# Kernel tuning notes

Measured on AMD Instinct MI355X. Metric: run time of the kernel, lower is better.

## Reference

```python
import jax, jax.numpy as jnp
import numpy as np

N = 100000   # nodes
E = 1000000  # edges per block
P = 100000   # pos/neg link edges
IN = 128
H = 64


def setup_inputs() -> dict:
    key = jax.random.key(0)
    ks = jax.random.split(key, 24)
    d = {}
    d["x"] = jax.random.normal(ks[0], (N, IN), jnp.float32)
    d["edge_weight"] = jax.random.uniform(ks[1], (3, E), jnp.float32)
    d["src"] = jax.random.randint(ks[2], (E,), 0, N)
    d["dst"] = jax.random.randint(ks[3], (E,), 0, N)
    d["pos_src"] = jax.random.randint(ks[4], (P,), 0, N)
    d["pos_dst"] = jax.random.randint(ks[5], (P,), 0, N)
    d["neg_src"] = jax.random.randint(ks[6], (P,), 0, N)
    d["neg_dst"] = jax.random.randint(ks[7], (P,), 0, N)
    s = 1.0 / np.sqrt(IN)
    h = 1.0 / np.sqrt(H)
    d["W0"] = jax.random.normal(ks[8], (IN, H), jnp.float32) * s
    d["b0"] = jnp.zeros((H,), jnp.float32)
    d["W1"] = jax.random.normal(ks[9], (H, H), jnp.float32) * h
    d["b1"] = jnp.zeros((H,), jnp.float32)
    d["W2"] = jax.random.normal(ks[10], (H, H), jnp.float32) * h
    d["b2"] = jnp.zeros((H,), jnp.float32)
    d["P0"] = jax.random.normal(ks[11], (H, H), jnp.float32) * h
    d["pb0"] = jnp.zeros((H,), jnp.float32)
    d["P1"] = jax.random.normal(ks[12], (H, H), jnp.float32) * h
    d["pb1"] = jnp.zeros((H,), jnp.float32)
    d["P2"] = jax.random.normal(ks[13], (H, 1), jnp.float32) * h
    d["pb2"] = jnp.zeros((1,), jnp.float32)
    return d


def _graph_conv(h, W, b, src, dst, ew, n_nodes):
    # DGL GraphConv, norm='both': D_out^{-1/2} on source feats,
    # edge-weighted sum aggregation, D_in^{-1/2} on result, then linear.
    ones = jnp.ones(src.shape[0], h.dtype)
    deg_out = jax.ops.segment_sum(ones, src, num_segments=n_nodes)
    deg_in = jax.ops.segment_sum(ones, dst, num_segments=n_nodes)
    norm_src = jax.lax.rsqrt(jnp.maximum(deg_out, 1.0))
    norm_dst = jax.lax.rsqrt(jnp.maximum(deg_in, 1.0))
    # apply weight before aggregation (in_feats >= out_feats); math-equivalent either way
    hw = (h * norm_src[:, None]) @ W            # [N, H]
    msg = hw[src] * ew[:, None]                 # [E, H] gather + scale
    agg = jax.ops.segment_sum(msg, dst, num_segments=n_nodes)  # scatter-add
    return agg * norm_dst[:, None] + b


def reference(x, edge_weight, src, dst, pos_src, pos_dst, neg_src, neg_dst,
              W0, b0, W1, b1, W2, b2, P0, pb0, P1, pb1, P2, pb2):
    h = jax.nn.relu(_graph_conv(x, W0, b0, src, dst, edge_weight[0], N))
    h = jax.nn.relu(_graph_conv(h, W1, b1, src, dst, edge_weight[1], N))
    h = _graph_conv(h, W2, b2, src, dst, edge_weight[2], N)  # no relu on last layer

    def mlp(z):
        z = jax.nn.relu(z @ P0 + pb0)
        z = jax.nn.relu(z @ P1 + pb1)
        return z @ P2 + pb2

    h_pos = mlp(h[pos_src] * h[pos_dst])  # [P, 1]
    h_neg = mlp(h[neg_src] * h[neg_dst])  # [P, 1]
    return (h_pos, h_neg)
```

## Files before the change

### kernel.cpp

```cpp
#include <hip/hip_runtime.h>


#define NN 100000
#define NE 1000000
#define NP 100000
#define SCAN_NB 98

__device__ __forceinline__ void row_fma(float4& acc, float xv, const float4& wv) {
    acc.x = fmaf(xv, wv.x, acc.x);
    acc.y = fmaf(xv, wv.y, acc.y);
    acc.z = fmaf(xv, wv.z, acc.z);
    acc.w = fmaf(xv, wv.w, acc.w);
}

__global__ void deg_kernel(const int4* __restrict__ src4, const int4* __restrict__ dst4,
                           int* __restrict__ deg_out, int* __restrict__ deg_in, int E4) {
    int tid = blockIdx.x * blockDim.x + threadIdx.x;
    if (tid < E4) {
        int4 s = src4[tid], d = dst4[tid];
        atomicAdd(&deg_out[s.x], 1);
        atomicAdd(&deg_out[s.y], 1);
        atomicAdd(&deg_out[s.z], 1);
        atomicAdd(&deg_out[s.w], 1);
        atomicAdd(&deg_in[d.x], 1);
        atomicAdd(&deg_in[d.y], 1);
        atomicAdd(&deg_in[d.z], 1);
        atomicAdd(&deg_in[d.w], 1);
    }
}

__global__ void norm_kernel(const int* __restrict__ deg_out, const int* __restrict__ deg_in,
                            float* __restrict__ norm_src, float* __restrict__ norm_dst, int n) {
    int i = blockIdx.x * blockDim.x + threadIdx.x;
    if (i < n) {
        norm_src[i] = rsqrtf(fmaxf((float)deg_out[i], 1.0f));
        norm_dst[i] = rsqrtf(fmaxf((float)deg_in[i], 1.0f));
    }
}

__global__ __launch_bounds__(1024) void scan_block(const int* __restrict__ deg,
                                                   int* __restrict__ tmp_excl,
                                                   int* __restrict__ blocksums, int n) {
    __shared__ int wsums[16];
    const int i = blockIdx.x * 1024 + threadIdx.x;
    const int lane = threadIdx.x & 63, w = threadIdx.x >> 6;
    int v = (i < n) ? deg[i] : 0;
    int s = v;
#pragma unroll
    for (int off = 1; off < 64; off <<= 1) {
        int u = __shfl_up(s, off, 64);
        if (lane >= off) s += u;
    }
    if (lane == 63) wsums[w] = s;
    __syncthreads();
    if (w == 0) {
        int wv = (lane < 16) ? wsums[lane] : 0;
#pragma unroll
        for (int off = 1; off < 16; off <<= 1) {
            int u = __shfl_up(wv, off, 64);
            if (lane >= off) wv += u;
        }
        if (lane < 16) wsums[lane] = wv;
    }
    __syncthreads();
    int excl = s - v + (w > 0 ? wsums[w - 1] : 0);
    if (i < n) tmp_excl[i] = excl;
    if (threadIdx.x == 1023) blocksums[blockIdx.x] = excl + v;
}

__global__ void scan_sums(int* __restrict__ bs, int nb) {
    __shared__ int wtot[2];
    const int t = threadIdx.x;
    const int lane = t & 63, w = t >> 6;
    int v = (t < nb) ? bs[t] : 0;
    int s = v;
#pragma unroll
    for (int off = 1; off < 64; off <<= 1) {
        int u = __shfl_up(s, off, 64);
        if (lane >= off) s += u;
    }
    if (lane == 63) wtot[w] = s;
    __syncthreads();
    int excl = s - v + (w == 1 ? wtot[0] : 0);
    if (t < nb) bs[t] = excl;
}

__global__ __launch_bounds__(1024) void scan_apply(const int* __restrict__ tmp_excl,
                                                   const int* __restrict__ bs,
                                                   int* __restrict__ row_ptr,
                                                   int* __restrict__ cursor, int n) {
    const int i = blockIdx.x * 1024 + threadIdx.x;
    if (i < n) {
        int r = tmp_excl[i] + bs[blockIdx.x];
        row_ptr[i] = r;
        cursor[i] = r;
    }
    if (i == 0) row_ptr[n] = NE;
}

__global__ void csr_fill(const int* __restrict__ src, const int* __restrict__ dst,
                         const float* __restrict__ ew, int* __restrict__ cursor,
                         float4* __restrict__ cedge, int E) {
    int tid = blockIdx.x * blockDim.x + threadIdx.x;
    int stride = gridDim.x * blockDim.x;
    for (int e = tid; e < E; e += stride) {
        int d = dst[e];
        int slot = atomicAdd(&cursor[d], 1);
        float4 c;
        c.x = __int_as_float(src[e]);
        c.y = ew[e];
        c.z = ew[NE + e];
        c.w = ew[2 * NE + e];
        cedge[slot] = c;
    }
}

template <int WSEL, bool FINAL>
__global__ __launch_bounds__(256) void aggregate(const float* __restrict__ hw,
                                                 const float4* __restrict__ cedge,
                                                 const int* __restrict__ row_ptr,
                                                 const float* __restrict__ norm_src,
                                                 const float* __restrict__ norm_dst,
                                                 const float* __restrict__ bias,
                                                 float* __restrict__ outx, int n) {
    const int lane = threadIdx.x & 63;
    const int gw = (blockIdx.x * blockDim.x + threadIdx.x) >> 6;
    const int nw = (gridDim.x * blockDim.x) >> 6;
    const float blane = bias[lane];
    for (int node = gw; node < n; node += nw) {
        int beg = row_ptr[node], end = row_ptr[node + 1];
        float a0 = 0.f, a1 = 0.f, a2 = 0.f, a3 = 0.f;
        int i = beg;
        for (; i + 7 < end; i += 8) {
            float4 c0 = cedge[i + 0], c1 = cedge[i + 1], c2 = cedge[i + 2], c3 = cedge[i + 3];
            float4 c4 = cedge[i + 4], c5 = cedge[i + 5], c6 = cedge[i + 6], c7 = cedge[i + 7];
            float h0 = hw[__float_as_int(c0.x) * 64 + lane];
            float h1 = hw[__float_as_int(c1.x) * 64 + lane];
            float h2 = hw[__float_as_int(c2.x) * 64 + lane];
            float h3 = hw[__float_as_int(c3.x) * 64 + lane];
            float h4 = hw[__float_as_int(c4.x) * 64 + lane];
            float h5 = hw[__float_as_int(c5.x) * 64 + lane];
            float h6 = hw[__float_as_int(c6.x) * 64 + lane];
            float h7 = hw[__float_as_int(c7.x) * 64 + lane];
            a0 = fmaf(h0, (WSEL == 0) ? c0.y : (WSEL == 1) ? c0.z : c0.w, a0);
            a1 = fmaf(h1, (WSEL == 0) ? c1.y : (WSEL == 1) ? c1.z : c1.w, a1);
            a2 = fmaf(h2, (WSEL == 0) ? c2.y : (WSEL == 1) ? c2.z : c2.w, a2);
            a3 = fmaf(h3, (WSEL == 0) ? c3.y : (WSEL == 1) ? c3.z : c3.w, a3);
            a0 = fmaf(h4, (WSEL == 0) ? c4.y : (WSEL == 1) ? c4.z : c4.w, a0);
            a1 = fmaf(h5, (WSEL == 0) ? c5.y : (WSEL == 1) ? c5.z : c5.w, a1);
            a2 = fmaf(h6, (WSEL == 0) ? c6.y : (WSEL == 1) ? c6.z : c6.w, a2);
            a3 = fmaf(h7, (WSEL == 0) ? c7.y : (WSEL == 1) ? c7.z : c7.w, a3);
        }
        for (; i + 1 < end; i += 2) {
            float4 c0 = cedge[i], c1 = cedge[i + 1];
            float h0 = hw[__float_as_int(c0.x) * 64 + lane];
            float h1 = hw[__float_as_int(c1.x) * 64 + lane];
            a0 = fmaf(h0, (WSEL == 0) ? c0.y : (WSEL == 1) ? c0.z : c0.w, a0);
            a1 = fmaf(h1, (WSEL == 0) ? c1.y : (WSEL == 1) ? c1.z : c1.w, a1);
        }
        if (i < end) {
            float4 c0 = cedge[i];
            float h0 = hw[__float_as_int(c0.x) * 64 + lane];
            a0 = fmaf(h0, (WSEL == 0) ? c0.y : (WSEL == 1) ? c0.z : c0.w, a0);
        }
        float a = (a0 + a1) + (a2 + a3);
        float nd = norm_dst[node];
        float t;
        if (FINAL) {
            t = fmaf(a, nd, blane);
        } else {
            t = fmaxf(fmaf(a, nd, blane), 0.f) * norm_src[node];
        }
        outx[node * 64 + lane] = t;
    }
}

template <int K, bool SCALE>
__global__ __launch_bounds__(256, 5) void gemm_tile(const float* __restrict__ in,
                                                    const float* __restrict__ W,
                                                    const float* __restrict__ norm_src,
                                                    float* __restrict__ out, int n) {
    __shared__ float Ws[K * 64];
    const int tid = threadIdx.x;
    for (int i = tid; i < K * 16; i += 256) ((float4*)Ws)[i] = ((const float4*)W)[i];
    __syncthreads();

    const int tr = tid >> 4, tc = tid & 15;
    const int row0 = blockIdx.x * 64 + tr * 4;
    const float* xr0 = in + (size_t)min(row0 + 0, n - 1) * K;
    const float* xr1 = in + (size_t)min(row0 + 1, n - 1) * K;
    const float* xr2 = in + (size_t)min(row0 + 2, n - 1) * K;
    const float* xr3 = in + (size_t)min(row0 + 3, n - 1) * K;

    float4 acc0 = {0, 0, 0, 0}, acc1 = {0, 0, 0, 0}, acc2 = {0, 0, 0, 0}, acc3 = {0, 0, 0, 0};
#pragma unroll 4
    for (int k4 = 0; k4 < K / 4; ++k4) {
        const int kb = k4 * 4;
        float4 xv0 = *(const float4*)&xr0[kb];
        float4 xv1 = *(const float4*)&xr1[kb];
        float4 xv2 = *(const float4*)&xr2[kb];
        float4 xv3 = *(const float4*)&xr3[kb];
        const float* wb = &Ws[kb * 64 + tc * 4];
        float4 wk;
        wk = *(const float4*)(wb);
        row_fma(acc0, xv0.x, wk); row_fma(acc1, xv1.x, wk); row_fma(acc2, xv2.x, wk); row_fma(acc3, xv3.x, wk);
        wk = *(const float4*)(wb + 64);
        row_fma(acc0, xv0.y, wk); row_fma(acc1, xv1.y, wk); row_fma(acc2, xv2.y, wk); row_fma(acc3, xv3.y, wk);
        wk = *(const float4*)(wb + 128);
        row_fma(acc0, xv0.z, wk); row_fma(acc1, xv1.z, wk); row_fma(acc2, xv2.z, wk); row_fma(acc3, xv3.z, wk);
        wk = *(const float4*)(wb + 192);
        row_fma(acc0, xv0.w, wk); row_fma(acc1, xv1.w, wk); row_fma(acc2, xv2.w, wk); row_fma(acc3, xv3.w, wk);
    }

#pragma unroll
    for (int i = 0; i < 4; ++i) {
        int row = row0 + i;
        if (row < n) {
            float4 o = (i == 0) ? acc0 : (i == 1) ? acc1 : (i == 2) ? acc2 : acc3;
            if (SCALE) {
                float ns = norm_src[row];
                o.x *= ns; o.y *= ns; o.z *= ns; o.w *= ns;
            }
            *(float4*)&out[row * 64 + tc * 4] = o;
        }
    }
}

#define ZST 76

__global__ __launch_bounds__(256) void mlp_tile(const float* __restrict__ hfin,
                                                const float* __restrict__ P0,
                                                const float* __restrict__ pb0,
                                                const float* __restrict__ P1,
                                                const float* __restrict__ pb1,
                                                const float* __restrict__ P2,
                                                const float* __restrict__ pb2,
                                                const int* __restrict__ pos_src,
                                                const int* __restrict__ pos_dst,
                                                const int* __restrict__ neg_src,
                                                const int* __restrict__ neg_dst,
                                                float* __restrict__ out, int P) {
    __shared__ float Zs[64][ZST];
    __shared__ float pb0s[64], pb1s[64], P2s[64];
    __shared__ int pas[64], pbs[64];
    const int tid = threadIdx.x;
    const int base = blockIdx.x << 6;
    if (tid < 64) {
        pb0s[tid] = pb0[tid];
        pb1s[tid] = pb1[tid];
        P2s[tid] = P2[tid];
        int p = base + tid;
        pas[tid] = (p < P) ? pos_src[p] : neg_src[p - P];
        pbs[tid] = (p < P) ? pos_dst[p] : neg_dst[p - P];
    }
    const float pb2v = pb2[0];
    const int lane = tid & 63, w = tid >> 6;
    const int tr = tid >> 4, tc = tid & 15;
    __syncthreads();

    {
        const int p0 = 0 + w, p1 = 4 + w, p2 = 8 + w, p3 = 12 + w;
#pragma unroll
        for (int pb = 0; pb < 64; pb += 16) {
            int a0 = pas[pb + p0], b0 = pbs[pb + p0];
            int a1 = pas[pb + p1], b1 = pbs[pb + p1];
            int a2 = pas[pb + p2], b2 = pbs[pb + p2];
            int a3 = pas[pb + p3], b3 = pbs[pb + p3];
            float ha0 = hfin[a0 * 64 + lane], hb0 = hfin[b0 * 64 + lane];
            float ha1 = hfin[a1 * 64 + lane], hb1 = hfin[b1 * 64 + lane];
            float ha2 = hfin[a2 * 64 + lane], hb2 = hfin[b2 * 64 + lane];
            float ha3 = hfin[a3 * 64 + lane], hb3 = hfin[b3 * 64 + lane];
            Zs[pb + p0][lane] = ha0 * hb0;
            Zs[pb + p1][lane] = ha1 * hb1;
            Zs[pb + p2][lane] = ha2 * hb2;
            Zs[pb + p3][lane] = ha3 * hb3;
        }
    }
    __syncthreads();

    float4 acc0, acc1, acc2, acc3;
    {
        float4 binit = *(const float4*)&pb0s[tc * 4];
        acc0 = binit; acc1 = binit; acc2 = binit; acc3 = binit;
    }
#pragma unroll 4
    for (int k4 = 0; k4 < 16; ++k4) {
        const int kb = k4 * 4;
        float4 xv0 = *(const float4*)&Zs[tr * 4 + 0][kb];
        float4 xv1 = *(const float4*)&Zs[tr * 4 + 1][kb];
        float4 xv2 = *(const float4*)&Zs[tr * 4 + 2][kb];
        float4 xv3 = *(const float4*)&Zs[tr * 4 + 3][kb];
        const float* wb = &P0[kb * 64 + tc * 4];
        float4 wk;
        wk = *(const float4*)(wb);
        row_fma(acc0, xv0.x, wk); row_fma(acc1, xv1.x, wk); row_fma(acc2, xv2.x, wk); row_fma(acc3, xv3.x, wk);
        wk = *(const float4*)(wb + 64);
        row_fma(acc0, xv0.y, wk); row_fma(acc1, xv1.y, wk); row_fma(acc2, xv2.y, wk); row_fma(acc3, xv3.y, wk);
        wk = *(const float4*)(wb + 128);
        row_fma(acc0, xv0.z, wk); row_fma(acc1, xv1.z, wk); row_fma(acc2, xv2.z, wk); row_fma(acc3, xv3.z, wk);
        wk = *(const float4*)(wb + 192);
        row_fma(acc0, xv0.w, wk); row_fma(acc1, xv1.w, wk); row_fma(acc2, xv2.w, wk); row_fma(acc3, xv3.w, wk);
    }
    __syncthreads();
#pragma unroll
    for (int i = 0; i < 4; ++i) {
        float4 o = (i == 0) ? acc0 : (i == 1) ? acc1 : (i == 2) ? acc2 : acc3;
        o.x = fmaxf(o.x, 0.f); o.y = fmaxf(o.y, 0.f); o.z = fmaxf(o.z, 0.f); o.w = fmaxf(o.w, 0.f);
        *(float4*)&Zs[tr * 4 + i][tc * 4] = o;
    }
    __syncthreads();

    {
        float4 binit = *(const float4*)&pb1s[tc * 4];
        acc0 = binit; acc1 = binit; acc2 = binit; acc3 = binit;
    }
#pragma unroll 4
    for (int k4 = 0; k4 < 16; ++k4) {
        const int kb = k4 * 4;
        float4 xv0 = *(const float4*)&Zs[tr * 4 + 0][kb];
        float4 xv1 = *(const float4*)&Zs[tr * 4 + 1][kb];
        float4 xv2 = *(const float4*)&Zs[tr * 4 + 2][kb];
        float4 xv3 = *(const float4*)&Zs[tr * 4 + 3][kb];
        const float* wb = &P1[kb * 64 + tc * 4];
        float4 wk;
        wk = *(const float4*)(wb);
        row_fma(acc0, xv0.x, wk); row_fma(acc1, xv1.x, wk); row_fma(acc2, xv2.x, wk); row_fma(acc3, xv3.x, wk);
        wk = *(const float4*)(wb + 64);
        row_fma(acc0, xv0.y, wk); row_fma(acc1, xv1.y, wk); row_fma(acc2, xv2.y, wk); row_fma(acc3, xv3.y, wk);
        wk = *(const float4*)(wb + 128);
        row_fma(acc0, xv0.z, wk); row_fma(acc1, xv1.z, wk); row_fma(acc2, xv2.z, wk); row_fma(acc3, xv3.z, wk);
        wk = *(const float4*)(wb + 192);
        row_fma(acc0, xv0.w, wk); row_fma(acc1, xv1.w, wk); row_fma(acc2, xv2.w, wk); row_fma(acc3, xv3.w, wk);
    }
    __syncthreads();
#pragma unroll
    for (int i = 0; i < 4; ++i) {
        float4 o = (i == 0) ? acc0 : (i == 1) ? acc1 : (i == 2) ? acc2 : acc3;
        o.x = fmaxf(o.x, 0.f); o.y = fmaxf(o.y, 0.f); o.z = fmaxf(o.z, 0.f); o.w = fmaxf(o.w, 0.f);
        *(float4*)&Zs[tr * 4 + i][tc * 4] = o;
    }
    __syncthreads();

    {
        int p = tid >> 2, kq = tid & 3;
        float s = 0.f;
#pragma unroll
        for (int i = 0; i < 16; ++i) s = fmaf(Zs[p][kq * 16 + i], P2s[kq * 16 + i], s);
        s += __shfl_xor(s, 1, 64);
        s += __shfl_xor(s, 2, 64);
        if (kq == 0) out[base + p] = s + pb2v;
    }
}

extern "C" void kernel_launch(void* const* d_in, const int* in_sizes, int n_in,
                              void* d_out, int out_size, void* d_ws, size_t ws_size,
                              hipStream_t stream) {
    const float* x     = (const float*)d_in[0];
    const float* ew    = (const float*)d_in[1];
    const int* src     = (const int*)d_in[2];
    const int* dst     = (const int*)d_in[3];
    const int* pos_src = (const int*)d_in[4];
    const int* pos_dst = (const int*)d_in[5];
    const int* neg_src = (const int*)d_in[6];
    const int* neg_dst = (const int*)d_in[7];
    const float* W0    = (const float*)d_in[8];
    const float* b0    = (const float*)d_in[9];
    const float* W1    = (const float*)d_in[10];
    const float* b1    = (const float*)d_in[11];
    const float* W2    = (const float*)d_in[12];
    const float* b2    = (const float*)d_in[13];
    const float* P0    = (const float*)d_in[14];
    const float* pb0   = (const float*)d_in[15];
    const float* P1    = (const float*)d_in[16];
    const float* pb1   = (const float*)d_in[17];
    const float* P2    = (const float*)d_in[18];
    const float* pb2   = (const float*)d_in[19];
    float* out = (float*)d_out;

    float* ws = (float*)d_ws;
    float* norm_src = ws;
    float* norm_dst = ws + 100000;
    int* cursor     = (int*)(ws + 200000);
    int* deg_in     = (int*)(ws + 300000);
    int* row_ptr    = (int*)(ws + 400000);
    float4* cedge   = (float4*)(ws + 500004);
    float* hw       = ws + 4500004;
    float* agg      = ws + 10900004;

    int* tmp_excl  = (int*)hw;
    int* blocksums = (int*)hw + NN;

    hipMemsetAsync(cursor, 0, 2 * NN * sizeof(int), stream);
    deg_kernel<<<(NE / 4 + 255) / 256, 256, 0, stream>>>((const int4*)src, (const int4*)dst,
                                                         cursor, deg_in, NE / 4);
    norm_kernel<<<(NN + 255) / 256, 256, 0, stream>>>(cursor, deg_in, norm_src, norm_dst, NN);
    scan_block<<<SCAN_NB, 1024, 0, stream>>>(deg_in, tmp_excl, blocksums, NN);
    scan_sums<<<1, 128, 0, stream>>>(blocksums, SCAN_NB);
    scan_apply<<<SCAN_NB, 1024, 0, stream>>>(tmp_excl, blocksums, row_ptr, cursor, NN);
    csr_fill<<<2048, 256, 0, stream>>>(src, dst, ew, cursor, cedge, NE);

    const int NT = (NN + 63) / 64;

    gemm_tile<128, true><<<NT, 256, 0, stream>>>(x, W0, norm_src, hw, NN);
    aggregate<0, false><<<4096, 256, 0, stream>>>(hw, cedge, row_ptr, norm_src, norm_dst, b0, agg, NN);
    gemm_tile<64, false><<<NT, 256, 0, stream>>>(agg, W1, nullptr, hw, NN);
    aggregate<1, false><<<4096, 256, 0, stream>>>(hw, cedge, row_ptr, norm_src, norm_dst, b1, agg, NN);
    gemm_tile<64, false><<<NT, 256, 0, stream>>>(agg, W2, nullptr, hw, NN);
    aggregate<2, true><<<4096, 256, 0, stream>>>(hw, cedge, row_ptr, norm_src, norm_dst, b2, agg, NN);

    mlp_tile<<<(2 * NP) / 64, 256, 0, stream>>>(agg, P0, pb0, P1, pb1, P2, pb2,
                                                pos_src, pos_dst, neg_src, neg_dst, out, NP);
}
```

Baseline: 484.2 us.

## Replicate degree histograms per XCC and widen MLP gather batching

Degree counting now reads the XCC id and writes into one of eight per-XCC replicas, using workgroup-scope relaxed atomics instead of device-scope ones. This is meant to cut cross-die atomic contention. A new kernel sums the replicas, computes both norms and writes deg_in for the scan. The MLP gather also changes: each wave now takes 16 consecutive pairs with eight pairs of loads in flight, to raise memory-level parallelism. The trade-offs are a larger memset and an extra reduction pass. Correctness also now depends on workgroup-scope atomics being coherent through the shared L2 within one XCC.

```diff
diff --git a/kernel.cpp b/kernel.cpp
--- a/kernel.cpp
+++ b/kernel.cpp
@@ -14,27 +14,39 @@
 }
 
 __global__ void deg_kernel(const int4* __restrict__ src4, const int4* __restrict__ dst4,
-                           int* __restrict__ deg_out, int* __restrict__ deg_in, int E4) {
+                           int* __restrict__ repl, int E4) {
+    int xcc;
+    asm volatile("s_getreg_b32 %0, hwreg(HW_REG_XCC_ID)" : "=s"(xcc));
+    xcc &= 7;
+    int* dout = repl + xcc * NN;
+    int* din  = repl + (8 + xcc) * NN;
     int tid = blockIdx.x * blockDim.x + threadIdx.x;
     if (tid < E4) {
         int4 s = src4[tid], d = dst4[tid];
-        atomicAdd(&deg_out[s.x], 1);
-        atomicAdd(&deg_out[s.y], 1);
-        atomicAdd(&deg_out[s.z], 1);
-        atomicAdd(&deg_out[s.w], 1);
-        atomicAdd(&deg_in[d.x], 1);
-        atomicAdd(&deg_in[d.y], 1);
-        atomicAdd(&deg_in[d.z], 1);
-        atomicAdd(&deg_in[d.w], 1);
-    }
-}
-
-__global__ void norm_kernel(const int* __restrict__ deg_out, const int* __restrict__ deg_in,
-                            float* __restrict__ norm_src, float* __restrict__ norm_dst, int n) {
+        __hip_atomic_fetch_add(&dout[s.x], 1, __ATOMIC_RELAXED, __HIP_MEMORY_SCOPE_WORKGROUP);
+        __hip_atomic_fetch_add(&dout[s.y], 1, __ATOMIC_RELAXED, __HIP_MEMORY_SCOPE_WORKGROUP);
+        __hip_atomic_fetch_add(&dout[s.z], 1, __ATOMIC_RELAXED, __HIP_MEMORY_SCOPE_WORKGROUP);
+        __hip_atomic_fetch_add(&dout[s.w], 1, __ATOMIC_RELAXED, __HIP_MEMORY_SCOPE_WORKGROUP);
+        __hip_atomic_fetch_add(&din[d.x], 1, __ATOMIC_RELAXED, __HIP_MEMORY_SCOPE_WORKGROUP);
+        __hip_atomic_fetch_add(&din[d.y], 1, __ATOMIC_RELAXED, __HIP_MEMORY_SCOPE_WORKGROUP);
+        __hip_atomic_fetch_add(&din[d.z], 1, __ATOMIC_RELAXED, __HIP_MEMORY_SCOPE_WORKGROUP);
+        __hip_atomic_fetch_add(&din[d.w], 1, __ATOMIC_RELAXED, __HIP_MEMORY_SCOPE_WORKGROUP);
+    }
+}
+
+__global__ void reduce_norm_kernel(const int* __restrict__ repl, float* __restrict__ norm_src,
+                                   float* __restrict__ norm_dst, int* __restrict__ deg_in, int n) {
     int i = blockIdx.x * blockDim.x + threadIdx.x;
     if (i < n) {
-        norm_src[i] = rsqrtf(fmaxf((float)deg_out[i], 1.0f));
-        norm_dst[i] = rsqrtf(fmaxf((float)deg_in[i], 1.0f));
+        int so = 0, si = 0;
+#pragma unroll
+        for (int x = 0; x < 8; ++x) {
+            so += repl[x * NN + i];
+            si += repl[(8 + x) * NN + i];
+        }
+        norm_src[i] = rsqrtf(fmaxf((float)so, 1.0f));
+        norm_dst[i] = rsqrtf(fmaxf((float)si, 1.0f));
+        deg_in[i] = si;
     }
 }
 
@@ -259,21 +271,34 @@
     __syncthreads();
 
     {
-        const int p0 = 0 + w, p1 = 4 + w, p2 = 8 + w, p3 = 12 + w;
-#pragma unroll
-        for (int pb = 0; pb < 64; pb += 16) {
-            int a0 = pas[pb + p0], b0 = pbs[pb + p0];
-            int a1 = pas[pb + p1], b1 = pbs[pb + p1];
-            int a2 = pas[pb + p2], b2 = pbs[pb + p2];
-            int a3 = pas[pb + p3], b3 = pbs[pb + p3];
+        const int pbase = w * 16;
+#pragma unroll
+        for (int r = 0; r < 2; ++r) {
+            const int p0 = pbase + r * 8;
+            int a0 = pas[p0 + 0], b0 = pbs[p0 + 0];
+            int a1 = pas[p0 + 1], b1 = pbs[p0 + 1];
+            int a2 = pas[p0 + 2], b2 = pbs[p0 + 2];
+            int a3 = pas[p0 + 3], b3 = pbs[p0 + 3];
+            int a4 = pas[p0 + 4], b4 = pbs[p0 + 4];
+            int a5 = pas[p0 + 5], b5 = pbs[p0 + 5];
+            int a6 = pas[p0 + 6], b6 = pbs[p0 + 6];
+            int a7 = pas[p0 + 7], b7 = pbs[p0 + 7];
             float ha0 = hfin[a0 * 64 + lane], hb0 = hfin[b0 * 64 + lane];
             float ha1 = hfin[a1 * 64 + lane], hb1 = hfin[b1 * 64 + lane];
             float ha2 = hfin[a2 * 64 + lane], hb2 = hfin[b2 * 64 + lane];
             float ha3 = hfin[a3 * 64 + lane], hb3 = hfin[b3 * 64 + lane];
-            Zs[pb + p0][lane] = ha0 * hb0;
-            Zs[pb + p1][lane] = ha1 * hb1;
-            Zs[pb + p2][lane] = ha2 * hb2;
-            Zs[pb + p3][lane] = ha3 * hb3;
+            float ha4 = hfin[a4 * 64 + lane], hb4 = hfin[b4 * 64 + lane];
+            float ha5 = hfin[a5 * 64 + lane], hb5 = hfin[b5 * 64 + lane];
+            float ha6 = hfin[a6 * 64 + lane], hb6 = hfin[b6 * 64 + lane];
+            float ha7 = hfin[a7 * 64 + lane], hb7 = hfin[b7 * 64 + lane];
+            Zs[p0 + 0][lane] = ha0 * hb0;
+            Zs[p0 + 1][lane] = ha1 * hb1;
+            Zs[p0 + 2][lane] = ha2 * hb2;
+            Zs[p0 + 3][lane] = ha3 * hb3;
+            Zs[p0 + 4][lane] = ha4 * hb4;
+            Zs[p0 + 5][lane] = ha5 * hb5;
+            Zs[p0 + 6][lane] = ha6 * hb6;
+            Zs[p0 + 7][lane] = ha7 * hb7;
         }
     }
     __syncthreads();
@@ -387,13 +412,14 @@
     float* hw       = ws + 4500004;
     float* agg      = ws + 10900004;
 
-    int* tmp_excl  = (int*)hw;
-    int* blocksums = (int*)hw + NN;
-
-    hipMemsetAsync(cursor, 0, 2 * NN * sizeof(int), stream);
+    int* repl      = (int*)hw;
+    int* tmp_excl  = (int*)hw + 16 * NN;
+    int* blocksums = (int*)hw + 17 * NN;
+
+    hipMemsetAsync(repl, 0, 16 * NN * sizeof(int), stream);
     deg_kernel<<<(NE / 4 + 255) / 256, 256, 0, stream>>>((const int4*)src, (const int4*)dst,
-                                                         cursor, deg_in, NE / 4);
-    norm_kernel<<<(NN + 255) / 256, 256, 0, stream>>>(cursor, deg_in, norm_src, norm_dst, NN);
+                                                         repl, NE / 4);
+    reduce_norm_kernel<<<(NN + 255) / 256, 256, 0, stream>>>(repl, norm_src, norm_dst, deg_in, NN);
     scan_block<<<SCAN_NB, 1024, 0, stream>>>(deg_in, tmp_excl, blocksums, NN);
     scan_sums<<<1, 128, 0, stream>>>(blocksums, SCAN_NB);
     scan_apply<<<SCAN_NB, 1024, 0, stream>>>(tmp_excl, blocksums, row_ptr, cursor, NN);
```

New measurement: 489.0 us. No clear change (+1.0%).
